# Kernel tuning notes

Hardware: AMD Instinct MI355X
Metric: run time of the kernel (lower is better)

The kernel has to match this reference:

```python
import jax, jax.numpy as jnp
import numpy as np

N_DIM = 256
N_HEAD = 8
HEAD_DIM = N_DIM // N_HEAD  # 32


def setup_inputs() -> dict:
    key = jax.random.key(0)
    k_x, k_wqkv, k_bqkv, k_wp, k_bp = jax.random.split(key, 5)
    B, T, C = 32, 512, N_DIM
    x = jax.random.normal(k_x, (B, T, C), dtype=jnp.float32)
    # nn.Linear default init ~ U(-1/sqrt(fan_in), 1/sqrt(fan_in)); use scaled normal for simplicity
    s = 1.0 / np.sqrt(C)
    W_qkv = jax.random.normal(k_wqkv, (C, 3 * C), dtype=jnp.float32) * s
    b_qkv = jax.random.normal(k_bqkv, (3 * C,), dtype=jnp.float32) * s
    W_proj = jax.random.normal(k_wp, (C, C), dtype=jnp.float32) * s
    b_proj = jax.random.normal(k_bp, (C,), dtype=jnp.float32) * s
    return {"x": x, "W_qkv": W_qkv, "b_qkv": b_qkv, "W_proj": W_proj, "b_proj": b_proj}


def reference(x, W_qkv, b_qkv, W_proj, b_proj):
    B, T, C = x.shape
    H, D = N_HEAD, HEAD_DIM
    qkv = jnp.einsum('btc,cf->btf', x, W_qkv) + b_qkv  # [B,T,3C]
    q, k, v = jnp.split(qkv, 3, axis=2)
    # [B,T,C] -> [B,H,T,D]
    q = q.reshape(B, T, H, D).transpose(0, 2, 1, 3)
    k = k.reshape(B, T, H, D).transpose(0, 2, 1, 3)
    v = v.reshape(B, T, H, D).transpose(0, 2, 1, 3)
    scale = 1.0 / jnp.sqrt(jnp.float32(D))
    scores = jnp.einsum('bhqd,bhkd->bhqk', q, k) * scale  # [B,H,T,T]
    causal = jnp.tril(jnp.ones((T, T), dtype=bool))
    scores = jnp.where(causal, scores, jnp.finfo(scores.dtype).min)
    attn = jax.nn.softmax(scores, axis=-1)
    out = jnp.einsum('bhqk,bhkd->bhqd', attn, v)  # [B,H,T,D]
    out = out.transpose(0, 2, 1, 3).reshape(B, T, C)
    return jnp.einsum('btc,cf->btf', out, W_proj) + b_proj
```

## Files before the change

### kernel.cpp

```cpp
#include <hip/hip_runtime.h>
#include <stdint.h>
#include <stddef.h>

#define NB 32
#define NT 512
#define NC 256
#define NH 8
#define ND 32
#define NQTOT (NB*NH*NT*ND)

typedef __attribute__((ext_vector_type(8))) short short8;
typedef __attribute__((ext_vector_type(4))) float f32x4;

__device__ __forceinline__ unsigned short f2bf(float f) {
    union { float f; unsigned u; } x; x.f = f;
    unsigned r = (x.u + 0x7FFFu + ((x.u >> 16) & 1u)) >> 16;
    return (unsigned short)r;
}

__global__ __launch_bounds__(256) void k_cvt_w2(const float* __restrict__ wqkv,
                                                unsigned short* __restrict__ wqkvT,
                                                const float* __restrict__ wproj,
                                                unsigned short* __restrict__ wprojT) {
    __shared__ float tile[32][33];
    int bid = blockIdx.x;
    const float* w; unsigned short* wt; int N, bx, by;
    if (bid < 192) { w = wqkv; wt = wqkvT; N = 768; bx = bid % 24; by = bid / 24; }
    else { bid -= 192; w = wproj; wt = wprojT; N = 256; bx = bid % 8; by = bid / 8; }
    const int K = 256;
    const int tx = threadIdx.x & 31;
    const int ty = threadIdx.x >> 5;
    const int n0 = bx * 32, k0 = by * 32;
#pragma unroll
    for (int dy = 0; dy < 4; ++dy)
        tile[ty + dy * 8][tx] = w[(size_t)(k0 + ty + dy * 8) * N + n0 + tx];
    __syncthreads();
#pragma unroll
    for (int dy = 0; dy < 4; ++dy)
        wt[(size_t)(n0 + ty + dy * 8) * K + k0 + tx] = f2bf(tile[tx][ty + dy * 8]);
}

template <int EPI>
__global__ __launch_bounds__(256) void k_gemm(const void* __restrict__ Av,
                                              const unsigned short* __restrict__ Bt,
                                              const float* __restrict__ bias,
                                              unsigned short* __restrict__ qkv,
                                              float* __restrict__ outf,
                                              int M, int N, int K) {
    __shared__ unsigned short Al[2][128][40];
    __shared__ unsigned short Bl[2][128][40];

    const int tid = threadIdx.x;
    const int lane = tid & 63;
    const int w = tid >> 6;
    const int wm = w >> 1, wn = w & 1;
    const int i16 = lane & 15, g = lane >> 4;

    const int nbm = M >> 7;
    const int bm = blockIdx.x % nbm;
    const int bn = blockIdx.x / nbm;
    const int m0 = bm << 7, n0 = bn << 7;

    const float* Af = (const float*)Av;
    const unsigned short* Ab = (const unsigned short*)Av;

    f32x4 acc[4][4];
    const f32x4 z4 = {0.f, 0.f, 0.f, 0.f};
#pragma unroll
    for (int a = 0; a < 4; a++)
#pragma unroll
        for (int b = 0; b < 4; b++) acc[a][b] = z4;

    const int row0 = tid >> 2;
    const int cr = tid & 3;

    float4 fa[2][2];
    short8 sa[2];
    short8 sb[2];

    auto LOAD = [&](int k0) {
#pragma unroll
        for (int h = 0; h < 2; ++h) {
            const int row = row0 + h * 64;
            if (EPI == 0) {
                const float* p = &Af[(size_t)(m0 + row) * K + k0 + cr * 8];
                fa[h][0] = *reinterpret_cast<const float4*>(p);
                fa[h][1] = *reinterpret_cast<const float4*>(p + 4);
            } else {
                sa[h] = *reinterpret_cast<const short8*>(&Ab[(size_t)(m0 + row) * K + k0 + cr * 8]);
            }
            sb[h] = *reinterpret_cast<const short8*>(&Bt[(size_t)(n0 + row) * K + k0 + cr * 8]);
        }
    };
    auto STORE = [&](int buf) {
#pragma unroll
        for (int h = 0; h < 2; ++h) {
            const int row = row0 + h * 64;
            if (EPI == 0) {
                short8 t;
                t[0] = (short)f2bf(fa[h][0].x); t[1] = (short)f2bf(fa[h][0].y);
                t[2] = (short)f2bf(fa[h][0].z); t[3] = (short)f2bf(fa[h][0].w);
                t[4] = (short)f2bf(fa[h][1].x); t[5] = (short)f2bf(fa[h][1].y);
                t[6] = (short)f2bf(fa[h][1].z); t[7] = (short)f2bf(fa[h][1].w);
                *reinterpret_cast<short8*>(&Al[buf][row][cr * 8]) = t;
            } else {
                *reinterpret_cast<short8*>(&Al[buf][row][cr * 8]) = sa[h];
            }
            *reinterpret_cast<short8*>(&Bl[buf][row][cr * 8]) = sb[h];
        }
    };

    LOAD(0);
    STORE(0);
    __syncthreads();

    const int nk = K >> 5;
    for (int it = 0; it < nk; ++it) {
        const int cur = it & 1;
        if (it + 1 < nk) LOAD((it + 1) << 5);

        short8 af[4], bf[4];
#pragma unroll
        for (int mi = 0; mi < 4; mi++)
            af[mi] = *reinterpret_cast<const short8*>(&Al[cur][wm * 64 + mi * 16 + i16][g * 8]);
#pragma unroll
        for (int ni = 0; ni < 4; ni++)
            bf[ni] = *reinterpret_cast<const short8*>(&Bl[cur][wn * 64 + ni * 16 + i16][g * 8]);
#pragma unroll
        for (int mi = 0; mi < 4; mi++)
#pragma unroll
            for (int ni = 0; ni < 4; ni++)
                acc[mi][ni] = __builtin_amdgcn_mfma_f32_16x16x32_bf16(af[mi], bf[ni], acc[mi][ni], 0, 0, 0);

        if (it + 1 < nk) STORE(cur ^ 1);
        __syncthreads();
    }

#pragma unroll
    for (int mi = 0; mi < 4; mi++) {
#pragma unroll
        for (int ni = 0; ni < 4; ni++) {
            const int col = n0 + wn * 64 + ni * 16 + i16;
            const float bv = bias[col];
#pragma unroll
            for (int r = 0; r < 4; r++) {
                const int rowg = m0 + wm * 64 + mi * 16 + g * 4 + r;
                const float v = acc[mi][ni][r] + bv;
                if (EPI == 0) {
                    const int which = col >> 8;
                    const int cc = col & 255;
                    const int h = cc >> 5, d = cc & 31;
                    const int bb = rowg >> 9, t = rowg & 511;
                    qkv[(size_t)which * NQTOT +
                        ((((size_t)bb * NH + h) * NT + t) * ND) + d] = f2bf(v);
                } else {
                    outf[(size_t)rowg * N + col] = v;
                }
            }
        }
    }
}

__global__ __launch_bounds__(256) void k_attn(const unsigned short* __restrict__ qkv,
                                              unsigned short* __restrict__ Ob) {
    __shared__ unsigned short Vt[32][512];
    __shared__ unsigned short Pl[4][16][72];

    const int tid = threadIdx.x;
    const int lane = tid & 63;
    const int w = tid >> 6;
    const int i16 = lane & 15, g = lane >> 4;

    const int half = blockIdx.x >> 8;
    const int bh = blockIdx.x & 255;
    const unsigned short* Qp = qkv + (size_t)bh * NT * ND;
    const unsigned short* Kp = qkv + (size_t)NQTOT + (size_t)bh * NT * ND;
    const unsigned short* Vp = qkv + (size_t)2 * NQTOT + (size_t)bh * NT * ND;

    const int qbase = half * 256 + w * 64;
    const int ktmax = half * 4 + w;
    const int npass = (half + 1) * 4;

    const int srow = tid >> 2;
    const int scr = tid & 3;

    for (int p = 0; p < npass; ++p) {
        short8 v = *reinterpret_cast<const short8*>(&Vp[(p * 64 + srow) * ND + scr * 8]);
#pragma unroll
        for (int j = 0; j < 8; j++) {
            const int swz = j ^ (scr << 1);
            Vt[scr * 8 + j][p * 64 + (srow & 7) + 8 * ((srow >> 3) ^ swz)] = (unsigned short)v[j];
        }
    }

    short8 qf[4];
#pragma unroll
    for (int s = 0; s < 4; s++)
        qf[s] = *reinterpret_cast<const short8*>(&Qp[(qbase + s * 16 + i16) * ND + g * 8]);

    const f32x4 z4 = {0.f, 0.f, 0.f, 0.f};
    f32x4 O[4][2];
    float m_[4], l_[4];
#pragma unroll
    for (int s = 0; s < 4; s++) {
        O[s][0] = z4; O[s][1] = z4; m_[s] = -3e38f; l_[s] = 0.f;
    }

    __syncthreads();

    const float scale2 = 0.17677669529663687f * 1.4426950408889634f;

    for (int kt = 0; kt <= ktmax; ++kt) {
        short8 kr[4];
#pragma unroll
        for (int kc = 0; kc < 4; kc++)
            kr[kc] = *reinterpret_cast<const short8*>(&Kp[(kt * 64 + kc * 16 + i16) * ND + g * 8]);
        short8 vf[2][2];
#pragma unroll
        for (int kc2 = 0; kc2 < 2; kc2++)
#pragma unroll
            for (int dh = 0; dh < 2; dh++) {
                const int dd = dh * 16 + i16;
                const int swzd = (dd & 7) ^ (((dd >> 3) & 3) << 1);
                vf[kc2][dh] = *reinterpret_cast<const short8*>(
                    &Vt[dd][kt * 64 + 8 * ((kc2 * 4 + g) ^ swzd)]);
            }

        const bool diag = (kt == ktmax);
#pragma unroll
        for (int sub = 0; sub < 4; ++sub) {
            float s[4][4];
#pragma unroll
            for (int kc = 0; kc < 4; kc++) {
                if (!diag || kc <= sub) {
                    f32x4 sv = __builtin_amdgcn_mfma_f32_16x16x32_bf16(kr[kc], qf[sub], z4, 0, 0, 0);
                    if (diag && kc == sub) {
#pragma unroll
                        for (int r = 0; r < 4; r++)
                            s[kc][r] = (g * 4 + r <= i16) ? sv[r] * scale2 : -3e38f;
                    } else {
#pragma unroll
                        for (int r = 0; r < 4; r++) s[kc][r] = sv[r] * scale2;
                    }
                } else {
#pragma unroll
                    for (int r = 0; r < 4; r++) s[kc][r] = -3e38f;
                }
            }

            float tm = fmaxf(fmaxf(fmaxf(s[0][0], s[0][1]), fmaxf(s[0][2], s[0][3])),
                             fmaxf(fmaxf(s[1][0], s[1][1]), fmaxf(s[1][2], s[1][3])));
            tm = fmaxf(tm, fmaxf(fmaxf(fmaxf(s[2][0], s[2][1]), fmaxf(s[2][2], s[2][3])),
                                 fmaxf(fmaxf(s[3][0], s[3][1]), fmaxf(s[3][2], s[3][3]))));
            tm = fmaxf(tm, __shfl_xor(tm, 16, 64));
            tm = fmaxf(tm, __shfl_xor(tm, 32, 64));
            const float nm = fmaxf(m_[sub], tm);
            const float fr = exp2f(m_[sub] - nm);
            m_[sub] = nm;
            float ps = 0.f;
#pragma unroll
            for (int kc = 0; kc < 4; kc++)
#pragma unroll
                for (int r = 0; r < 4; r++) {
                    s[kc][r] = exp2f(s[kc][r] - nm);
                    ps += s[kc][r];
                }
            ps += __shfl_xor(ps, 16, 64);
            ps += __shfl_xor(ps, 32, 64);
            l_[sub] = l_[sub] * fr + ps;
            O[sub][0] *= fr; O[sub][1] *= fr;

#pragma unroll
            for (int kc = 0; kc < 4; kc++) {
                ushort4 pk;
                pk.x = f2bf(s[kc][0]); pk.y = f2bf(s[kc][1]);
                pk.z = f2bf(s[kc][2]); pk.w = f2bf(s[kc][3]);
                *reinterpret_cast<ushort4*>(&Pl[w][i16][kc * 16 + g * 4]) = pk;
            }
            asm volatile("s_waitcnt lgkmcnt(0)" ::: "memory");
            __builtin_amdgcn_sched_barrier(0);

#pragma unroll
            for (int kc2 = 0; kc2 < 2; kc2++) {
                short8 pf = *reinterpret_cast<const short8*>(&Pl[w][i16][kc2 * 32 + g * 8]);
                O[sub][0] = __builtin_amdgcn_mfma_f32_16x16x32_bf16(vf[kc2][0], pf, O[sub][0], 0, 0, 0);
                O[sub][1] = __builtin_amdgcn_mfma_f32_16x16x32_bf16(vf[kc2][1], pf, O[sub][1], 0, 0, 0);
            }
        }
    }

    const int b = bh >> 3, h = bh & 7;
#pragma unroll
    for (int sub = 0; sub < 4; ++sub) {
        const float inv = 1.f / l_[sub];
        const int q = qbase + sub * 16 + i16;
        const size_t base = ((size_t)(b * NT + q)) * NC + h * 32;
        ushort4 o0, o1;
        o0.x = f2bf(O[sub][0][0] * inv); o0.y = f2bf(O[sub][0][1] * inv);
        o0.z = f2bf(O[sub][0][2] * inv); o0.w = f2bf(O[sub][0][3] * inv);
        o1.x = f2bf(O[sub][1][0] * inv); o1.y = f2bf(O[sub][1][1] * inv);
        o1.z = f2bf(O[sub][1][2] * inv); o1.w = f2bf(O[sub][1][3] * inv);
        *reinterpret_cast<ushort4*>(&Ob[base + g * 4]) = o0;
        *reinterpret_cast<ushort4*>(&Ob[base + 16 + g * 4]) = o1;
    }
}

extern "C" void kernel_launch(void* const* d_in, const int* in_sizes, int n_in,
                              void* d_out, int out_size, void* d_ws, size_t ws_size,
                              hipStream_t stream) {
    const float* x     = (const float*)d_in[0];
    const float* Wqkv  = (const float*)d_in[1];
    const float* bqkv  = (const float*)d_in[2];
    const float* Wproj = (const float*)d_in[3];
    const float* bproj = (const float*)d_in[4];
    float* out = (float*)d_out;

    unsigned short* WqkvT  = (unsigned short*)d_ws;
    unsigned short* WprojT = WqkvT + (size_t)768 * 256;
    unsigned short* QKV    = WprojT + (size_t)256 * 256;
    unsigned short* Ob     = QKV + (size_t)3 * NQTOT;

    k_cvt_w2<<<256, 256, 0, stream>>>(Wqkv, WqkvT, Wproj, WprojT);

    k_gemm<0><<<128 * 6, 256, 0, stream>>>(x, WqkvT, bqkv, QKV, nullptr, 16384, 768, 256);
    k_attn<<<512, 256, 0, stream>>>(QKV, Ob);
    k_gemm<1><<<128 * 2, 256, 0, stream>>>(Ob, WprojT, bproj, nullptr, out, 16384, 256, 256);
}
```

Measured before the change: 129.5 us.

## Convert x to bf16 in prep kernel and load GEMM fragments directly from global

Moves the fp32-to-bf16 conversion of x into the prep kernel, writing a bf16 copy to workspace. The GEMM drops its LDS double-buffered staging: each wave loads its A and B MFMA fragments straight from global memory, with tiles changed to 256x64 per block and 64 rows per wave, relying on L1/L2 for reuse. This removes LDS traffic and barriers, but adds an extra pass over x and makes cross-wave reuse of B depend on the caches.

```diff
diff --git a/kernel.cpp b/kernel.cpp
--- a/kernel.cpp
+++ b/kernel.cpp
@@ -18,12 +18,26 @@
     return (unsigned short)r;
 }
 
-__global__ __launch_bounds__(256) void k_cvt_w2(const float* __restrict__ wqkv,
-                                                unsigned short* __restrict__ wqkvT,
-                                                const float* __restrict__ wproj,
-                                                unsigned short* __restrict__ wprojT) {
+__global__ __launch_bounds__(256) void k_prep(const float* __restrict__ x,
+                                              unsigned short* __restrict__ xb,
+                                              const float* __restrict__ wqkv,
+                                              unsigned short* __restrict__ wqkvT,
+                                              const float* __restrict__ wproj,
+                                              unsigned short* __restrict__ wprojT) {
+    int bid = blockIdx.x;
+    if (bid >= 256) {
+        const int i = ((bid - 256) * 256 + threadIdx.x) * 8;
+        const float4 v0 = *reinterpret_cast<const float4*>(&x[i]);
+        const float4 v1 = *reinterpret_cast<const float4*>(&x[i + 4]);
+        short8 t;
+        t[0] = (short)f2bf(v0.x); t[1] = (short)f2bf(v0.y);
+        t[2] = (short)f2bf(v0.z); t[3] = (short)f2bf(v0.w);
+        t[4] = (short)f2bf(v1.x); t[5] = (short)f2bf(v1.y);
+        t[6] = (short)f2bf(v1.z); t[7] = (short)f2bf(v1.w);
+        *reinterpret_cast<short8*>(&xb[i]) = t;
+        return;
+    }
     __shared__ float tile[32][33];
-    int bid = blockIdx.x;
     const float* w; unsigned short* wt; int N, bx, by;
     if (bid < 192) { w = wqkv; wt = wqkvT; N = 768; bx = bid % 24; by = bid / 24; }
     else { bid -= 192; w = wproj; wt = wprojT; N = 256; bx = bid % 8; by = bid / 8; }
@@ -41,28 +55,22 @@
 }
 
 template <int EPI>
-__global__ __launch_bounds__(256) void k_gemm(const void* __restrict__ Av,
+__global__ __launch_bounds__(256) void k_gemm(const unsigned short* __restrict__ A,
                                               const unsigned short* __restrict__ Bt,
                                               const float* __restrict__ bias,
                                               unsigned short* __restrict__ qkv,
                                               float* __restrict__ outf,
-                                              int M, int N, int K) {
-    __shared__ unsigned short Al[2][128][40];
-    __shared__ unsigned short Bl[2][128][40];
-
+                                              int M, int N) {
     const int tid = threadIdx.x;
     const int lane = tid & 63;
     const int w = tid >> 6;
-    const int wm = w >> 1, wn = w & 1;
     const int i16 = lane & 15, g = lane >> 4;
 
-    const int nbm = M >> 7;
+    const int nbm = M >> 8;
     const int bm = blockIdx.x % nbm;
     const int bn = blockIdx.x / nbm;
-    const int m0 = bm << 7, n0 = bn << 7;
-
-    const float* Af = (const float*)Av;
-    const unsigned short* Ab = (const unsigned short*)Av;
+    const int m0 = (bm << 8) + w * 64;
+    const int n0 = bn << 6;
 
     f32x4 acc[4][4];
     const f32x4 z4 = {0.f, 0.f, 0.f, 0.f};
@@ -71,80 +79,39 @@
 #pragma unroll
         for (int b = 0; b < 4; b++) acc[a][b] = z4;
 
-    const int row0 = tid >> 2;
-    const int cr = tid & 3;
-
-    float4 fa[2][2];
-    short8 sa[2];
-    short8 sb[2];
-
-    auto LOAD = [&](int k0) {
-#pragma unroll
-        for (int h = 0; h < 2; ++h) {
-            const int row = row0 + h * 64;
-            if (EPI == 0) {
-                const float* p = &Af[(size_t)(m0 + row) * K + k0 + cr * 8];
-                fa[h][0] = *reinterpret_cast<const float4*>(p);
-                fa[h][1] = *reinterpret_cast<const float4*>(p + 4);
-            } else {
-                sa[h] = *reinterpret_cast<const short8*>(&Ab[(size_t)(m0 + row) * K + k0 + cr * 8]);
-            }
-            sb[h] = *reinterpret_cast<const short8*>(&Bt[(size_t)(n0 + row) * K + k0 + cr * 8]);
-        }
-    };
-    auto STORE = [&](int buf) {
-#pragma unroll
-        for (int h = 0; h < 2; ++h) {
-            const int row = row0 + h * 64;
-            if (EPI == 0) {
-                short8 t;
-                t[0] = (short)f2bf(fa[h][0].x); t[1] = (short)f2bf(fa[h][0].y);
-                t[2] = (short)f2bf(fa[h][0].z); t[3] = (short)f2bf(fa[h][0].w);
-                t[4] = (short)f2bf(fa[h][1].x); t[5] = (short)f2bf(fa[h][1].y);
-                t[6] = (short)f2bf(fa[h][1].z); t[7] = (short)f2bf(fa[h][1].w);
-                *reinterpret_cast<short8*>(&Al[buf][row][cr * 8]) = t;
-            } else {
-                *reinterpret_cast<short8*>(&Al[buf][row][cr * 8]) = sa[h];
-            }
-            *reinterpret_cast<short8*>(&Bl[buf][row][cr * 8]) = sb[h];
-        }
-    };
-
-    LOAD(0);
-    STORE(0);
-    __syncthreads();
-
-    const int nk = K >> 5;
-    for (int it = 0; it < nk; ++it) {
-        const int cur = it & 1;
-        if (it + 1 < nk) LOAD((it + 1) << 5);
-
-        short8 af[4], bf[4];
-#pragma unroll
-        for (int mi = 0; mi < 4; mi++)
-            af[mi] = *reinterpret_cast<const short8*>(&Al[cur][wm * 64 + mi * 16 + i16][g * 8]);
+#pragma unroll
+    for (int kh = 0; kh < 2; ++kh) {
+        short8 bfr[4][4];
 #pragma unroll
         for (int ni = 0; ni < 4; ni++)
-            bf[ni] = *reinterpret_cast<const short8*>(&Bl[cur][wn * 64 + ni * 16 + i16][g * 8]);
-#pragma unroll
-        for (int mi = 0; mi < 4; mi++)
-#pragma unroll
-            for (int ni = 0; ni < 4; ni++)
-                acc[mi][ni] = __builtin_amdgcn_mfma_f32_16x16x32_bf16(af[mi], bf[ni], acc[mi][ni], 0, 0, 0);
-
-        if (it + 1 < nk) STORE(cur ^ 1);
-        __syncthreads();
+#pragma unroll
+            for (int k2 = 0; k2 < 4; k2++)
+                bfr[ni][k2] = *reinterpret_cast<const short8*>(
+                    &Bt[(size_t)(n0 + ni * 16 + i16) * 256 + kh * 128 + k2 * 32 + g * 8]);
+#pragma unroll
+        for (int k2 = 0; k2 < 4; k2++) {
+            short8 af[4];
+#pragma unroll
+            for (int mi = 0; mi < 4; mi++)
+                af[mi] = *reinterpret_cast<const short8*>(
+                    &A[(size_t)(m0 + mi * 16 + i16) * 256 + kh * 128 + k2 * 32 + g * 8]);
+#pragma unroll
+            for (int mi = 0; mi < 4; mi++)
+#pragma unroll
+                for (int ni = 0; ni < 4; ni++)
+                    acc[mi][ni] = __builtin_amdgcn_mfma_f32_16x16x32_bf16(af[mi], bfr[ni][k2], acc[mi][ni], 0, 0, 0);
+        }
     }
 
 #pragma unroll
     for (int mi = 0; mi < 4; mi++) {
 #pragma unroll
         for (int ni = 0; ni < 4; ni++) {
-            const int col = n0 + wn * 64 + ni * 16 + i16;
+            const int col = n0 + ni * 16 + i16;
             const float bv = bias[col];
 #pragma unroll
             for (int r = 0; r < 4; r++) {
-                const int rowg = m0 + wm * 64 + mi * 16 + g * 4 + r;
+                const int rowg = m0 + mi * 16 + g * 4 + r;
                 const float v = acc[mi][ni][r] + bv;
                 if (EPI == 0) {
                     const int which = col >> 8;
@@ -315,14 +282,15 @@
     const float* bproj = (const float*)d_in[4];
     float* out = (float*)d_out;
 
-    unsigned short* WqkvT  = (unsigned short*)d_ws;
+    unsigned short* Xb     = (unsigned short*)d_ws;
+    unsigned short* WqkvT  = Xb + (size_t)16384 * 256;
     unsigned short* WprojT = WqkvT + (size_t)768 * 256;
     unsigned short* QKV    = WprojT + (size_t)256 * 256;
     unsigned short* Ob     = QKV + (size_t)3 * NQTOT;
 
-    k_cvt_w2<<<256, 256, 0, stream>>>(Wqkv, WqkvT, Wproj, WprojT);
-
-    k_gemm<0><<<128 * 6, 256, 0, stream>>>(x, WqkvT, bqkv, QKV, nullptr, 16384, 768, 256);
+    k_prep<<<2304, 256, 0, stream>>>(x, Xb, Wqkv, WqkvT, Wproj, WprojT);
+
+    k_gemm<0><<<64 * 12, 256, 0, stream>>>(Xb, WqkvT, bqkv, QKV, nullptr, 16384, 768);
     k_attn<<<512, 256, 0, stream>>>(QKV, Ob);
-    k_gemm<1><<<128 * 2, 256, 0, stream>>>(Ob, WprojT, bproj, nullptr, out, 16384, 256, 256);
-}
+    k_gemm<1><<<64 * 4, 256, 0, stream>>>(Ob, WprojT, bproj, nullptr, out, 16384, 256);
+}
```

Result: slower. 145.0 us (+12.0%).
